# Optimization experiments

Measured on AMD Instinct MI355X. Metric: run time of the kernel, lower is better.

The kernel has to match this reference:

```python
import jax, jax.numpy as jnp
import numpy as np

N = 50000        # nodes
E = 800000       # edges (avg degree 16)
F_IN = 128       # num_node_features
HEADS = 4        # const.NUM_HEADS
CH = 32          # const.NUM_CHANNELS
CLS = 40         # num_classes
NEG_SLOPE = 0.2  # PyG GATv2Conv default


def setup_inputs() -> dict:
    key = jax.random.key(0)
    ks = jax.random.split(key, 10)
    x = jax.random.normal(ks[0], (N, F_IN), dtype=jnp.float32)
    edge_index = jax.random.randint(ks[1], (2, E), 0, N, dtype=jnp.int64)
    s1 = 1.0 / np.sqrt(F_IN)
    s2 = 1.0 / np.sqrt(HEADS * CH)
    w1_l = jax.random.normal(ks[2], (F_IN, HEADS * CH), jnp.float32) * s1
    w1_r = jax.random.normal(ks[3], (F_IN, HEADS * CH), jnp.float32) * s1
    a1 = jax.random.normal(ks[4], (HEADS, CH), jnp.float32) * (1.0 / np.sqrt(CH))
    b1 = jnp.zeros((HEADS * CH,), jnp.float32)
    w2_l = jax.random.normal(ks[5], (HEADS * CH, CLS), jnp.float32) * s2
    w2_r = jax.random.normal(ks[6], (HEADS * CH, CLS), jnp.float32) * s2
    a2 = jax.random.normal(ks[7], (1, CLS), jnp.float32) * (1.0 / np.sqrt(CLS))
    b2 = jnp.zeros((CLS,), jnp.float32)
    return {"x": x, "edge_index": edge_index, "w1_l": w1_l, "w1_r": w1_r,
            "a1": a1, "b1": b1, "w2_l": w2_l, "w2_r": w2_r, "a2": a2, "b2": b2}


def _gatv2_conv(x, src, dst, wl, wr, a, b, concat):
    """GATv2Conv (PyG semantics, eval mode: no dropout).
    src -> lin_l, dst -> lin_r; e = a . LeakyReLU(x_l[src] + x_r[dst]);
    segment softmax over dst; out_i = sum_j alpha * x_l[src]."""
    H, C = a.shape
    n = x.shape[0]
    xl = (x @ wl).reshape(n, H, C)
    xr = (x @ wr).reshape(n, H, C)
    # per-edge additive attention logits [E, H]
    e = jnp.einsum('ehc,hc->eh', jax.nn.leaky_relu(xl[src] + xr[dst], NEG_SLOPE), a)
    # numerically stable segment softmax over target nodes
    m = jax.ops.segment_max(e, dst, num_segments=n)          # [n, H]
    p = jnp.exp(e - m[dst])
    denom = jax.ops.segment_sum(p, dst, num_segments=n)     # [n, H]
    alpha = p / denom[dst]
    out = jax.ops.segment_sum(alpha[..., None] * xl[src], dst, num_segments=n)  # [n, H, C]
    out = out.reshape(n, H * C) if concat else out.mean(axis=1)
    return out + b


def reference(x, edge_index, w1_l, w1_r, a1, b1, w2_l, w2_r, a2, b2):
    n = x.shape[0]
    # PyG GATv2Conv default add_self_loops=True
    loop = jnp.arange(n, dtype=edge_index.dtype)
    src = jnp.concatenate([edge_index[0], loop])
    dst = jnp.concatenate([edge_index[1], loop])
    h = jax.nn.elu(_gatv2_conv(x, src, dst, w1_l, w1_r, a1, b1, concat=True))
    # F.dropout with training=False is identity
    out = _gatv2_conv(h, src, dst, w2_l, w2_r, a2, b2, concat=False)
    return jax.nn.log_softmax(out, axis=1)
```

## Files before the change

kernel.cpp:

```cpp
#include <hip/hip_runtime.h>
#include <hip/hip_bf16.h>
#include <math.h>

#define NN 50000
#define NE 800000
#define ETOT (NE + NN)
#define CLS 40
#define CLSP 48
#define NEG 0.2f
#define MTILES (NN / 16)
#define GB1 ((MTILES + 3) / 4)
#define PREPB 176
#define NBUCK 196
#define BCAP 8192
#define EB 4096
#define KAB ((ETOT + EB - 1) / EB)
#define NHALF (NN / 2)

#define L2E 1.44269504088896f
#define C06 (0.6f * L2E)
#define C04 (0.4f * L2E)

typedef __hip_bfloat16 bf16;
typedef __attribute__((ext_vector_type(8))) __bf16 bf16x8;
typedef __attribute__((ext_vector_type(4))) float f32x4;
typedef __attribute__((ext_vector_type(2))) float f32x2;
struct U3 { unsigned x, y, z; };

__device__ __forceinline__ bf16x8 cvt8(f32x4 a, f32x4 b) {
    bf16x8 r;
    r[0] = (__bf16)a[0]; r[1] = (__bf16)a[1]; r[2] = (__bf16)a[2]; r[3] = (__bf16)a[3];
    r[4] = (__bf16)b[0]; r[5] = (__bf16)b[1]; r[6] = (__bf16)b[2]; r[7] = (__bf16)b[3];
    return r;
}
__device__ __forceinline__ f32x2 unpk2(unsigned u) {
    f32x2 r;
    r.x = __uint_as_float(u << 16);
    r.y = __uint_as_float(u & 0xffff0000u);
    return r;
}

__device__ __forceinline__ unsigned scan256(unsigned v, unsigned* wsum) {
    int t = threadIdx.x;
    int lane = t & 63, w = t >> 6;
    unsigned inc = v;
#pragma unroll
    for (int d = 1; d < 64; d <<= 1) {
        unsigned x = __shfl_up(inc, d);
        if (lane >= d) inc += x;
    }
    if (lane == 63) wsum[w] = inc;
    __syncthreads();
    unsigned woff = 0;
#pragma unroll
    for (int i = 0; i < 4; i++) woff += (i < w) ? wsum[i] : 0;
    return woff + inc - v;
}

__global__ __launch_bounds__(256) void prep(
        const float* __restrict__ w1l, const float* __restrict__ w1r,
        const float* __restrict__ w2l, const float* __restrict__ w2r,
        bf16* __restrict__ wT1, bf16* __restrict__ wT2,
        int* __restrict__ bcursor) {
    int t = blockIdx.x * 256 + threadIdx.x;
    if (t < NBUCK) bcursor[t] = 0;
    if (t < 2 * 128 * 128) {
        int m = t >> 14;
        int idx = t & 16383;
        int n = idx >> 7, k = idx & 127;
        const float* w = m ? w1r : w1l;
        wT1[t] = __float2bfloat16(w[k * 128 + n]);
    } else if (t < 2 * 128 * 128 + 2 * CLSP * 128) {
        int u = t - 2 * 128 * 128;
        int m = u / (CLSP * 128);
        int idx = u % (CLSP * 128);
        int n = idx >> 7, k = idx & 127;
        const float* w = m ? w2r : w2l;
        wT2[u] = __float2bfloat16((n < CLS) ? w[k * CLS + n] : 0.0f);
    }
}

__global__ __launch_bounds__(256) void gemm1_scatter(
        const float* __restrict__ x, const bf16* __restrict__ wT,
        bf16* __restrict__ outL, bf16* __restrict__ outR,
        const int* __restrict__ ei, int* __restrict__ bcursor,
        uint2* __restrict__ tmp) {
    __shared__ unsigned hist[256];
    __shared__ unsigned lstart[256];
    __shared__ unsigned lcur[256];
    __shared__ unsigned gbase[256];
    __shared__ unsigned wsum[4];
    __shared__ uint2 binned[EB];
    __shared__ unsigned target[EB];
    if ((int)blockIdx.x < GB1) {
        int wave = threadIdx.x >> 6;
        int lane = threadIdx.x & 63;
        int tile = blockIdx.x * 4 + wave;
        if (tile >= MTILES) return;
        const bf16* wl = wT;
        const bf16* wr = wT + 128 * 128;
        int row0 = tile * 16;
        int l16 = lane & 15, quad = lane >> 4;
        f32x4 z = {0.f, 0.f, 0.f, 0.f};
        f32x4 accl[8], accr[8];
#pragma unroll
        for (int i = 0; i < 8; i++) { accl[i] = z; accr[i] = z; }
        const float* xrow = x + (size_t)(row0 + l16) * 128 + quad * 8;
#pragma unroll
        for (int k0 = 0; k0 < 128; k0 += 32) {
            f32x4 a0 = *reinterpret_cast<const f32x4*>(xrow + k0);
            f32x4 a1v = *reinterpret_cast<const f32x4*>(xrow + k0 + 4);
            bf16x8 a = cvt8(a0, a1v);
#pragma unroll
            for (int ct = 0; ct < 8; ct++) {
                bf16x8 bl = *reinterpret_cast<const bf16x8*>(wl + (ct * 16 + l16) * 128 + k0 + quad * 8);
                bf16x8 br = *reinterpret_cast<const bf16x8*>(wr + (ct * 16 + l16) * 128 + k0 + quad * 8);
                accl[ct] = __builtin_amdgcn_mfma_f32_16x16x32_bf16(a, bl, accl[ct], 0, 0, 0);
                accr[ct] = __builtin_amdgcn_mfma_f32_16x16x32_bf16(a, br, accr[ct], 0, 0, 0);
            }
        }
#pragma unroll
        for (int ct = 0; ct < 8; ct++)
#pragma unroll
            for (int r = 0; r < 4; r++) {
                size_t o = (size_t)(row0 + quad * 4 + r) * 128 + ct * 16 + l16;
                outL[o] = __float2bfloat16(accl[ct][r]);
                outR[o] = __float2bfloat16(accr[ct][r]);
            }
    } else {
        int t = threadIdx.x;
        int e0 = (blockIdx.x - GB1) * EB;
        hist[t] = 0;
        __syncthreads();
        int srcs[16], dsts[16];
#pragma unroll
        for (int i = 0; i < 16; i++) {
            int e = e0 + i * 256 + t;
            if (e < ETOT) {
                int s, d;
                if (e < NE) { s = ei[e]; d = ei[NE + e]; }
                else        { s = d = e - NE; }
                srcs[i] = s; dsts[i] = d;
                atomicAdd(&hist[d >> 8], 1u);
            } else dsts[i] = -1;
        }
        __syncthreads();
        unsigned v = hist[t];
        unsigned excl = scan256(v, wsum);
        lstart[t] = excl;
        lcur[t] = 0;
        __syncthreads();
        if (t < NBUCK && v > 0)
            gbase[t] = (unsigned)atomicAdd(&bcursor[t], (int)v) + (unsigned)t * BCAP;
        __syncthreads();
#pragma unroll
        for (int i = 0; i < 16; i++) {
            int d = dsts[i];
            if (d >= 0) {
                int bk = d >> 8;
                unsigned p = atomicAdd(&lcur[bk], 1u);
                unsigned slot = lstart[bk] + p;
                binned[slot] = make_uint2((unsigned)srcs[i], (unsigned)d);
                target[slot] = gbase[bk] + p;
            }
        }
        __syncthreads();
        int tot = min(EB, ETOT - e0);
        for (int s = t; s < tot; s += 256)
            tmp[target[s]] = binned[s];
    }
}

__global__ __launch_bounds__(256) void bucket_sort(const int* __restrict__ bcursor,
                                                   const uint2* __restrict__ tmp,
                                                   int* __restrict__ csr_src,
                                                   int* __restrict__ startA,
                                                   int* __restrict__ degA) {
    __shared__ unsigned hist[256];
    __shared__ unsigned lcur[256];
    __shared__ unsigned wsum[4];
    __shared__ int vals[BCAP];
    int b = blockIdx.x, t = threadIdx.x;
    int cnt = bcursor[b];
    hist[t] = 0;
    __syncthreads();
    const uint2* seg = tmp + (size_t)b * BCAP;
    for (int s = t; s < cnt; s += 256)
        atomicAdd(&hist[seg[s].y & 255], 1u);
    __syncthreads();
    unsigned v = hist[t];
    unsigned excl = scan256(v, wsum);
    lcur[t] = excl;
    int node = b * 256 + t;
    if (node < NN) {
        startA[node] = b * BCAP + (int)excl;
        degA[node] = (int)v;
    }
    __syncthreads();
    for (int s = t; s < cnt; s += 256) {
        uint2 p = seg[s];
        unsigned pos = atomicAdd(&lcur[p.y & 255], 1u);
        vals[pos] = (int)p.x;
    }
    __syncthreads();
    int* cbase = csr_src + (size_t)b * BCAP;
    for (int s = t; s < cnt; s += 256)
        cbase[s] = vals[s];
}

struct L1S { float s; f32x2 acc[4]; };
__device__ __forceinline__ void l1_consume(uint4 u, bool valid, const f32x2* xrp,
                                           const f32x2* a06, const float* a04, L1S& st) {
    f32x2 t0 = unpk2(u.x) + xrp[0];
    f32x2 t1 = unpk2(u.y) + xrp[1];
    f32x2 t2 = unpk2(u.z) + xrp[2];
    f32x2 t3 = unpk2(u.w) + xrp[3];
    f32x2 ep = t0 * a06[0];
    ep = __builtin_elementwise_fma(t1, a06[1], ep);
    ep = __builtin_elementwise_fma(t2, a06[2], ep);
    ep = __builtin_elementwise_fma(t3, a06[3], ep);
    float e0 = fmaf(a04[1], fabsf(t0.y), a04[0] * fabsf(t0.x));
    e0 = fmaf(a04[2], fabsf(t1.x), e0);
    e0 = fmaf(a04[3], fabsf(t1.y), e0);
    float e1 = fmaf(a04[5], fabsf(t2.y), a04[4] * fabsf(t2.x));
    e1 = fmaf(a04[6], fabsf(t3.x), e1);
    e1 = fmaf(a04[7], fabsf(t3.y), e1);
    float e = (ep.x + ep.y) + (e0 + e1);
    e += __shfl_xor(e, 1);
    e += __shfl_xor(e, 2);
    float w = valid ? __builtin_amdgcn_exp2f(e) : 0.f;
    st.s += w;
    f32x2 wv = {w, w};
    st.acc[0] = __builtin_elementwise_fma(wv, t0, st.acc[0]);
    st.acc[1] = __builtin_elementwise_fma(wv, t1, st.acc[1]);
    st.acc[2] = __builtin_elementwise_fma(wv, t2, st.acc[2]);
    st.acc[3] = __builtin_elementwise_fma(wv, t3, st.acc[3]);
}

__global__ __launch_bounds__(256) void node_l1(const int* __restrict__ startA,
                                               const int* __restrict__ degA,
                                               const int* __restrict__ csr_src,
                                               const bf16* __restrict__ xl,
                                               const bf16* __restrict__ xr,
                                               const float* __restrict__ a1,
                                               const float* __restrict__ b1,
                                               bf16* __restrict__ hb,
                                               int nbase) {
    int wid = nbase + ((blockIdx.x * 256 + threadIdx.x) >> 6);
    int lane = threadIdx.x & 63;
    int g = lane >> 4, t = lane & 15;
    unsigned cB = (unsigned)t * 16;
    int j0 = startA[wid];
    int deg = degA[wid];
    unsigned rowB = (unsigned)csr_src[j0 + min(lane, deg - 1)] << 8;
    const char* xlb = (const char*)xl;
    f32x2 xrp[4];
    {
        uint4 raw = *(const uint4*)((const char*)xr + ((unsigned)wid << 8) + cB);
        xrp[0] = unpk2(raw.x); xrp[1] = unpk2(raw.y);
        xrp[2] = unpk2(raw.z); xrp[3] = unpk2(raw.w);
    }
    f32x2 a06[4];
    float a04[8];
    {
        f32x4 lo = *reinterpret_cast<const f32x4*>(a1 + t * 8);
        f32x4 hi = *reinterpret_cast<const f32x4*>(a1 + t * 8 + 4);
        float af[8];
#pragma unroll
        for (int k = 0; k < 4; k++) { af[k] = lo[k]; af[k + 4] = hi[k]; }
#pragma unroll
        for (int j = 0; j < 4; j++) {
            a06[j].x = af[2 * j] * C06;
            a06[j].y = af[2 * j + 1] * C06;
        }
#pragma unroll
        for (int k = 0; k < 8; k++) a04[k] = af[k] * C04;
    }
    L1S st; st.s = 0.f;
    f32x2 z2 = {0.f, 0.f};
#pragma unroll
    for (int k = 0; k < 4; k++) st.acc[k] = z2;
    int nb = (deg + 3) >> 2;
    uint4 u[8];
#pragma unroll
    for (int i = 0; i < 4; i++) {
        int pp = min(i * 4 + g, deg - 1);
        u[i] = *(const uint4*)(xlb + (__shfl(rowB, pp) + cB));
    }
    if (nb > 4) {
#pragma unroll
        for (int i = 4; i < 8; i++) {
            int pp = min(i * 4 + g, deg - 1);
            u[i] = *(const uint4*)(xlb + (__shfl(rowB, pp) + cB));
        }
    }
    l1_consume(u[0], g < deg, xrp, a06, a04, st);
    if (nb > 1) l1_consume(u[1], 4 + g < deg, xrp, a06, a04, st);
    if (nb > 2) l1_consume(u[2], 8 + g < deg, xrp, a06, a04, st);
    if (nb > 3) l1_consume(u[3], 12 + g < deg, xrp, a06, a04, st);
    if (nb > 4) {
        l1_consume(u[4], 16 + g < deg, xrp, a06, a04, st);
        if (nb > 5) l1_consume(u[5], 20 + g < deg, xrp, a06, a04, st);
        if (nb > 6) l1_consume(u[6], 24 + g < deg, xrp, a06, a04, st);
        if (nb > 7) l1_consume(u[7], 28 + g < deg, xrp, a06, a04, st);
        for (int b = 8; b < nb; b++) {
            int p = b * 4 + g;
            bool valid = p < deg;
            int pp = valid ? p : deg - 1;
            unsigned o = __shfl(rowB, min(pp, 63)) + cB;
            if (pp >= 64) o = (((unsigned)csr_src[j0 + pp]) << 8) + cB;
            uint4 uu = *(const uint4*)(xlb + o);
            l1_consume(uu, valid, xrp, a06, a04, st);
        }
    }
#pragma unroll
    for (int d = 16; d < 64; d <<= 1) {
        st.s += __shfl_xor(st.s, d);
#pragma unroll
        for (int k = 0; k < 4; k++) {
            st.acc[k].x += __shfl_xor(st.acc[k].x, d);
            st.acc[k].y += __shfl_xor(st.acc[k].y, d);
        }
    }
    if (g == 0) {
        float inv = 1.f / st.s;
        unsigned pk[4];
#pragma unroll
        for (int k = 0; k < 4; k++) {
            float o0 = st.acc[k].x * inv - xrp[k].x + b1[t * 8 + 2 * k];
            float o1 = st.acc[k].y * inv - xrp[k].y + b1[t * 8 + 2 * k + 1];
            o0 = o0 > 0.f ? o0 : __expf(o0) - 1.f;
            o1 = o1 > 0.f ? o1 : __expf(o1) - 1.f;
            bf16 r0 = __float2bfloat16(o0), r1 = __float2bfloat16(o1);
            pk[k] = (unsigned)*reinterpret_cast<unsigned short*>(&r0) |
                    ((unsigned)*reinterpret_cast<unsigned short*>(&r1) << 16);
        }
        uint4 w4 = {pk[0], pk[1], pk[2], pk[3]};
        *(uint4*)((char*)hb + ((unsigned)wid << 8) + cB) = w4;
    }
}

__global__ __launch_bounds__(256) void gemm2(const bf16* __restrict__ h,
                                             const bf16* __restrict__ wT,
                                             bf16* __restrict__ outL,
                                             bf16* __restrict__ outR) {
    int wave = threadIdx.x >> 6;
    int lane = threadIdx.x & 63;
    int tile = blockIdx.x * 4 + wave;
    if (tile >= MTILES) return;
    const bf16* wl = wT;
    const bf16* wr = wT + CLSP * 128;
    int row0 = tile * 16;
    int l16 = lane & 15, quad = lane >> 4;
    f32x4 z = {0.f, 0.f, 0.f, 0.f};
    f32x4 accl[3], accr[3];
#pragma unroll
    for (int i = 0; i < 3; i++) { accl[i] = z; accr[i] = z; }
    const bf16* hrow = h + (size_t)(row0 + l16) * 128 + quad * 8;
#pragma unroll
    for (int k0 = 0; k0 < 128; k0 += 32) {
        bf16x8 a = *reinterpret_cast<const bf16x8*>(hrow + k0);
#pragma unroll
        for (int ct = 0; ct < 3; ct++) {
            bf16x8 bl = *reinterpret_cast<const bf16x8*>(wl + (ct * 16 + l16) * 128 + k0 + quad * 8);
            bf16x8 br = *reinterpret_cast<const bf16x8*>(wr + (ct * 16 + l16) * 128 + k0 + quad * 8);
            accl[ct] = __builtin_amdgcn_mfma_f32_16x16x32_bf16(a, bl, accl[ct], 0, 0, 0);
            accr[ct] = __builtin_amdgcn_mfma_f32_16x16x32_bf16(a, br, accr[ct], 0, 0, 0);
        }
    }
#pragma unroll
    for (int ct = 0; ct < 3; ct++)
#pragma unroll
        for (int r = 0; r < 4; r++) {
            size_t o = (size_t)(row0 + quad * 4 + r) * CLSP + ct * 16 + l16;
            outL[o] = __float2bfloat16(accl[ct][r]);
            outR[o] = __float2bfloat16(accr[ct][r]);
        }
}

struct L2S { float s; f32x2 acc[3]; };
__device__ __forceinline__ void l2_consume(U3 u, bool valid, const f32x2* xrp,
                                           const f32x2* a06, const float* a04, L2S& st) {
    f32x2 t0 = unpk2(u.x) + xrp[0];
    f32x2 t1 = unpk2(u.y) + xrp[1];
    f32x2 t2 = unpk2(u.z) + xrp[2];
    f32x2 ep = t0 * a06[0];
    ep = __builtin_elementwise_fma(t1, a06[1], ep);
    ep = __builtin_elementwise_fma(t2, a06[2], ep);
    float es = fmaf(a04[1], fabsf(t0.y), a04[0] * fabsf(t0.x));
    es = fmaf(a04[2], fabsf(t1.x), es);
    es = fmaf(a04[3], fabsf(t1.y), es);
    es = fmaf(a04[4], fabsf(t2.x), es);
    es = fmaf(a04[5], fabsf(t2.y), es);
    float e = (ep.x + ep.y) + es;
    e += __shfl_xor(e, 1);
    e += __shfl_xor(e, 2);
    e += __shfl_xor(e, 4);
    float w = valid ? __builtin_amdgcn_exp2f(e) : 0.f;
    st.s += w;
    f32x2 wv = {w, w};
    st.acc[0] = __builtin_elementwise_fma(wv, t0, st.acc[0]);
    st.acc[1] = __builtin_elementwise_fma(wv, t1, st.acc[1]);
    st.acc[2] = __builtin_elementwise_fma(wv, t2, st.acc[2]);
}

__global__ __launch_bounds__(256) void node_l2(const int* __restrict__ startA,
                                               const int* __restrict__ degA,
                                               const int* __restrict__ csr_src,
                                               const bf16* __restrict__ xl2,
                                               const bf16* __restrict__ xr2,
                                               const float* __restrict__ a2,
                                               const float* __restrict__ b2,
                                               float* __restrict__ out) {
    int wid = (blockIdx.x * 256 + threadIdx.x) >> 6;
    int lane = threadIdx.x & 63;
    int g = lane >> 3, t = lane & 7;
    unsigned cB = (unsigned)t * 12;
    int j0 = startA[wid];
    int deg = degA[wid];
    unsigned rowB = (unsigned)csr_src[j0 + min(lane, deg - 1)] * 96u;
    const char* xlb = (const char*)xl2;
    f32x2 xrp[3];
    {
        U3 raw = *(const U3*)((const char*)xr2 + (unsigned)wid * 96u + cB);
        xrp[0] = unpk2(raw.x); xrp[1] = unpk2(raw.y); xrp[2] = unpk2(raw.z);
    }
    int c = t * 6;
    f32x2 a06[3];
    float a04[6];
#pragma unroll
    for (int k = 0; k < 6; k++) {
        float av = (c + k < CLS) ? a2[c + k] : 0.f;
        a04[k] = av * C04;
        if (k & 1) a06[k >> 1].y = av * C06; else a06[k >> 1].x = av * C06;
    }
    L2S st; st.s = 0.f;
    f32x2 z2 = {0.f, 0.f};
#pragma unroll
    for (int k = 0; k < 3; k++) st.acc[k] = z2;
    int nb = (deg + 7) >> 3;
    U3 u[4];
#pragma unroll
    for (int i = 0; i < 2; i++) {
        int pp = min(i * 8 + g, deg - 1);
        u[i] = *(const U3*)(xlb + (__shfl(rowB, pp) + cB));
    }
    if (nb > 2) {
#pragma unroll
        for (int i = 2; i < 4; i++) {
            int pp = min(i * 8 + g, deg - 1);
            u[i] = *(const U3*)(xlb + (__shfl(rowB, pp) + cB));
        }
    }
    l2_consume(u[0], g < deg, xrp, a06, a04, st);
    if (nb > 1) l2_consume(u[1], 8 + g < deg, xrp, a06, a04, st);
    if (nb > 2) {
        l2_consume(u[2], 16 + g < deg, xrp, a06, a04, st);
        if (nb > 3) l2_consume(u[3], 24 + g < deg, xrp, a06, a04, st);
        for (int b = 4; b < nb; b++) {
            int p = b * 8 + g;
            bool valid = p < deg;
            int pp = valid ? p : deg - 1;
            unsigned o = __shfl(rowB, min(pp, 63)) + cB;
            if (pp >= 64) o = (unsigned)csr_src[j0 + pp] * 96u + cB;
            U3 uu = *(const U3*)(xlb + o);
            l2_consume(uu, valid, xrp, a06, a04, st);
        }
    }
#pragma unroll
    for (int d = 8; d < 64; d <<= 1) {
        st.s += __shfl_xor(st.s, d);
#pragma unroll
        for (int k = 0; k < 3; k++) {
            st.acc[k].x += __shfl_xor(st.acc[k].x, d);
            st.acc[k].y += __shfl_xor(st.acc[k].y, d);
        }
    }
    float inv = 1.f / st.s;
    float q[6];
    float mx = -3e38f;
#pragma unroll
    for (int k = 0; k < 6; k++) {
        bool val = (c + k < CLS);
        float av = (k & 1) ? st.acc[k >> 1].y : st.acc[k >> 1].x;
        float xv = (k & 1) ? xrp[k >> 1].y : xrp[k >> 1].x;
        q[k] = val ? (av * inv - xv + b2[c + k]) : -3e38f;
        mx = fmaxf(mx, q[k]);
    }
    mx = fmaxf(mx, __shfl_xor(mx, 1));
    mx = fmaxf(mx, __shfl_xor(mx, 2));
    mx = fmaxf(mx, __shfl_xor(mx, 4));
    float se = 0.f;
#pragma unroll
    for (int k = 0; k < 6; k++) if (c + k < CLS) se += __expf(q[k] - mx);
    se += __shfl_xor(se, 1);
    se += __shfl_xor(se, 2);
    se += __shfl_xor(se, 4);
    float ls = mx + __logf(se);
    if (g == 0) {
        float* o = out + (size_t)wid * CLS + c;
#pragma unroll
        for (int k = 0; k < 6; k++)
            if (c + k < CLS) o[k] = q[k] - ls;
    }
}

extern "C" void kernel_launch(void* const* d_in, const int* in_sizes, int n_in,
                              void* d_out, int out_size, void* d_ws, size_t ws_size,
                              hipStream_t stream) {
    const float* x   = (const float*)d_in[0];
    const int*   ei  = (const int*)d_in[1];
    const float* w1l = (const float*)d_in[2];
    const float* w1r = (const float*)d_in[3];
    const float* a1  = (const float*)d_in[4];
    const float* b1  = (const float*)d_in[5];
    const float* w2l = (const float*)d_in[6];
    const float* w2r = (const float*)d_in[7];
    const float* a2  = (const float*)d_in[8];
    const float* b2  = (const float*)d_in[9];
    float* out = (float*)d_out;

    char* base = (char*)d_ws;
    int*   bcursor = (int*)(base + 0);
    int*   startA  = (int*)(base + 1024);
    int*   degA    = (int*)(base + 201024);
    uint2* tmp     = (uint2*)(base + 401024);
    int*   csr_src = (int*)(base + 13246080);
    bf16*  xl1     = (bf16*)(base + 19668608);
    bf16*  hb      = (bf16*)(base + 45268608);
    bf16*  xl2p    = (bf16*)(base + 58068608);
    bf16*  wT1     = (bf16*)(base + 67668608);
    bf16*  wT2     = (bf16*)(base + 67734144);
    bf16* xr1  = xl1 + (size_t)NN * 128;
    bf16* xr2p = xl2p + (size_t)NN * CLSP;

    prep<<<PREPB, 256, 0, stream>>>(w1l, w1r, w2l, w2r, wT1, wT2, bcursor);
    gemm1_scatter<<<GB1 + KAB, 256, 0, stream>>>(x, wT1, xl1, xr1, ei, bcursor, tmp);
    bucket_sort<<<NBUCK, 256, 0, stream>>>(bcursor, tmp, csr_src, startA, degA);
    node_l1<<<(NHALF * 64) / 256, 256, 0, stream>>>(startA, degA, csr_src, xl1, xr1, a1, b1, hb, 0);
    node_l1<<<(NHALF * 64) / 256, 256, 0, stream>>>(startA, degA, csr_src, xl1, xr1, a1, b1, hb, NHALF);
    gemm2<<<GB1, 256, 0, stream>>>(hb, wT2, xl2p, xr2p);
    node_l2<<<(NN * 64) / 256, 256, 0, stream>>>(startA, degA, csr_src, xl2p, xr2p, a2, b2, out);
}
```

Baseline: 232.1 us.

## Replace bucket sort CSR build with global atomic count, scan, scatter

Replaces the two-level bucketed sort (shared-memory binning plus per-bucket local sort) with a classic CSR build: per-node atomic degree counting fused into the first GEMM launch, a single-block prefix scan, and a global-atomic scatter of source ids. This drops the large intermediate tmp buffer and the per-block shared-memory histogramming, at the cost of global atomic contention and a serial single-block scan kernel. CSR order within a node becomes nondeterministic, which may change floating-point summation order. It also splits node_l2 into two half launches.

Result: slower. 313.9 us (+35.3%).

```diff
diff --git a/kernel.cpp b/kernel.cpp
--- a/kernel.cpp
+++ b/kernel.cpp
@@ -5,16 +5,15 @@
 #define NN 50000
 #define NE 800000
 #define ETOT (NE + NN)
+#define NPAD 50176
 #define CLS 40
 #define CLSP 48
 #define NEG 0.2f
 #define MTILES (NN / 16)
 #define GB1 ((MTILES + 3) / 4)
-#define PREPB 176
-#define NBUCK 196
-#define BCAP 8192
-#define EB 4096
-#define KAB ((ETOT + EB - 1) / EB)
+#define PREPB 196
+#define CNTB 196
+#define SCB 208
 #define NHALF (NN / 2)
 
 #define L2E 1.44269504088896f
@@ -61,9 +60,9 @@
         const float* __restrict__ w1l, const float* __restrict__ w1r,
         const float* __restrict__ w2l, const float* __restrict__ w2r,
         bf16* __restrict__ wT1, bf16* __restrict__ wT2,
-        int* __restrict__ bcursor) {
+        int* __restrict__ degA) {
     int t = blockIdx.x * 256 + threadIdx.x;
-    if (t < NBUCK) bcursor[t] = 0;
+    if (t < NPAD) degA[t] = (t < NN) ? 1 : 0;
     if (t < 2 * 128 * 128) {
         int m = t >> 14;
         int idx = t & 16383;
@@ -80,18 +79,10 @@
     }
 }
 
-__global__ __launch_bounds__(256) void gemm1_scatter(
+__global__ __launch_bounds__(256) void gemm1_count(
         const float* __restrict__ x, const bf16* __restrict__ wT,
         bf16* __restrict__ outL, bf16* __restrict__ outR,
-        const int* __restrict__ ei, int* __restrict__ bcursor,
-        uint2* __restrict__ tmp) {
-    __shared__ unsigned hist[256];
-    __shared__ unsigned lstart[256];
-    __shared__ unsigned lcur[256];
-    __shared__ unsigned gbase[256];
-    __shared__ unsigned wsum[4];
-    __shared__ uint2 binned[EB];
-    __shared__ unsigned target[EB];
+        const int* __restrict__ ei, int* __restrict__ degA) {
     if ((int)blockIdx.x < GB1) {
         int wave = threadIdx.x >> 6;
         int lane = threadIdx.x & 63;
@@ -129,83 +120,59 @@
             }
     } else {
         int t = threadIdx.x;
-        int e0 = (blockIdx.x - GB1) * EB;
-        hist[t] = 0;
-        __syncthreads();
-        int srcs[16], dsts[16];
+        int e0 = ((int)blockIdx.x - GB1) * 4096;
 #pragma unroll
         for (int i = 0; i < 16; i++) {
             int e = e0 + i * 256 + t;
-            if (e < ETOT) {
-                int s, d;
-                if (e < NE) { s = ei[e]; d = ei[NE + e]; }
-                else        { s = d = e - NE; }
-                srcs[i] = s; dsts[i] = d;
-                atomicAdd(&hist[d >> 8], 1u);
-            } else dsts[i] = -1;
-        }
-        __syncthreads();
-        unsigned v = hist[t];
-        unsigned excl = scan256(v, wsum);
-        lstart[t] = excl;
-        lcur[t] = 0;
-        __syncthreads();
-        if (t < NBUCK && v > 0)
-            gbase[t] = (unsigned)atomicAdd(&bcursor[t], (int)v) + (unsigned)t * BCAP;
-        __syncthreads();
-#pragma unroll
-        for (int i = 0; i < 16; i++) {
-            int d = dsts[i];
-            if (d >= 0) {
-                int bk = d >> 8;
-                unsigned p = atomicAdd(&lcur[bk], 1u);
-                unsigned slot = lstart[bk] + p;
-                binned[slot] = make_uint2((unsigned)srcs[i], (unsigned)d);
-                target[slot] = gbase[bk] + p;
-            }
-        }
-        __syncthreads();
-        int tot = min(EB, ETOT - e0);
-        for (int s = t; s < tot; s += 256)
-            tmp[target[s]] = binned[s];
-    }
-}
-
-__global__ __launch_bounds__(256) void bucket_sort(const int* __restrict__ bcursor,
-                                                   const uint2* __restrict__ tmp,
-                                                   int* __restrict__ csr_src,
-                                                   int* __restrict__ startA,
-                                                   int* __restrict__ degA) {
-    __shared__ unsigned hist[256];
-    __shared__ unsigned lcur[256];
+            if (e < NE) atomicAdd(&degA[ei[NE + e]], 1);
+        }
+    }
+}
+
+__global__ __launch_bounds__(256) void scan_deg(const int* __restrict__ degA,
+                                                int* __restrict__ startA,
+                                                int* __restrict__ cursor) {
     __shared__ unsigned wsum[4];
-    __shared__ int vals[BCAP];
-    int b = blockIdx.x, t = threadIdx.x;
-    int cnt = bcursor[b];
-    hist[t] = 0;
-    __syncthreads();
-    const uint2* seg = tmp + (size_t)b * BCAP;
-    for (int s = t; s < cnt; s += 256)
-        atomicAdd(&hist[seg[s].y & 255], 1u);
-    __syncthreads();
-    unsigned v = hist[t];
-    unsigned excl = scan256(v, wsum);
-    lcur[t] = excl;
-    int node = b * 256 + t;
-    if (node < NN) {
-        startA[node] = b * BCAP + (int)excl;
-        degA[node] = (int)v;
-    }
-    __syncthreads();
-    for (int s = t; s < cnt; s += 256) {
-        uint2 p = seg[s];
-        unsigned pos = atomicAdd(&lcur[p.y & 255], 1u);
-        vals[pos] = (int)p.x;
-    }
-    __syncthreads();
-    int* cbase = csr_src + (size_t)b * BCAP;
-    for (int s = t; s < cnt; s += 256)
-        cbase[s] = vals[s];
+    int t = threadIdx.x;
+    const int4* d4 = reinterpret_cast<const int4*>(degA) + t * 49;
+    int s = 0;
+#pragma unroll 7
+    for (int i = 0; i < 49; i++) {
+        int4 v = d4[i];
+        s += v.x + v.y + v.z + v.w;
+    }
+    int run = (int)scan256((unsigned)s, wsum);
+    int4* s4 = reinterpret_cast<int4*>(startA) + t * 49;
+    int4* c4 = reinterpret_cast<int4*>(cursor) + t * 49;
+#pragma unroll 7
+    for (int i = 0; i < 49; i++) {
+        int4 v = d4[i];
+        int4 o;
+        o.x = run; run += v.x;
+        o.y = run; run += v.y;
+        o.z = run; run += v.z;
+        o.w = run; run += v.w;
+        s4[i] = o;
+        c4[i] = o;
+    }
+}
+
+__global__ __launch_bounds__(256) void scatter(const int* __restrict__ ei,
+                                               int* __restrict__ cursor,
+                                               int* __restrict__ csr_src) {
+    int t = threadIdx.x;
+    int e0 = blockIdx.x * 4096;
+#pragma unroll
+    for (int i = 0; i < 16; i++) {
+        int e = e0 + i * 256 + t;
+        if (e < ETOT) {
+            int s, d;
+            if (e < NE) { s = ei[e]; d = ei[NE + e]; }
+            else        { s = d = e - NE; }
+            int pos = atomicAdd(&cursor[d], 1);
+            csr_src[pos] = s;
+        }
+    }
 }
 
 struct L1S { float s; f32x2 acc[4]; };
@@ -411,8 +378,9 @@
                                                const bf16* __restrict__ xr2,
                                                const float* __restrict__ a2,
                                                const float* __restrict__ b2,
-                                               float* __restrict__ out) {
-    int wid = (blockIdx.x * 256 + threadIdx.x) >> 6;
+                                               float* __restrict__ out,
+                                               int nbase) {
+    int wid = nbase + ((blockIdx.x * 256 + threadIdx.x) >> 6);
     int lane = threadIdx.x & 63;
     int g = lane >> 3, t = lane & 7;
     unsigned cB = (unsigned)t * 12;
@@ -521,24 +489,25 @@
     float* out = (float*)d_out;
 
     char* base = (char*)d_ws;
-    int*   bcursor = (int*)(base + 0);
-    int*   startA  = (int*)(base + 1024);
-    int*   degA    = (int*)(base + 201024);
-    uint2* tmp     = (uint2*)(base + 401024);
-    int*   csr_src = (int*)(base + 13246080);
-    bf16*  xl1     = (bf16*)(base + 19668608);
-    bf16*  hb      = (bf16*)(base + 45268608);
-    bf16*  xl2p    = (bf16*)(base + 58068608);
-    bf16*  wT1     = (bf16*)(base + 67668608);
-    bf16*  wT2     = (bf16*)(base + 67734144);
+    int*   startA  = (int*)(base + 0);
+    int*   degA    = (int*)(base + 200704);
+    int*   cursor  = (int*)(base + 401408);
+    int*   csr_src = (int*)(base + 602112);
+    bf16*  xl1     = (bf16*)(base + 4002112);
+    bf16*  hb      = (bf16*)(base + 29602112);
+    bf16*  xl2p    = (bf16*)(base + 42402112);
+    bf16*  wT1     = (bf16*)(base + 52002112);
+    bf16*  wT2     = (bf16*)(base + 52067648);
     bf16* xr1  = xl1 + (size_t)NN * 128;
     bf16* xr2p = xl2p + (size_t)NN * CLSP;
 
-    prep<<<PREPB, 256, 0, stream>>>(w1l, w1r, w2l, w2r, wT1, wT2, bcursor);
-    gemm1_scatter<<<GB1 + KAB, 256, 0, stream>>>(x, wT1, xl1, xr1, ei, bcursor, tmp);
-    bucket_sort<<<NBUCK, 256, 0, stream>>>(bcursor, tmp, csr_src, startA, degA);
+    prep<<<PREPB, 256, 0, stream>>>(w1l, w1r, w2l, w2r, wT1, wT2, degA);
+    gemm1_count<<<GB1 + CNTB, 256, 0, stream>>>(x, wT1, xl1, xr1, ei, degA);
+    scan_deg<<<1, 256, 0, stream>>>(degA, startA, cursor);
+    scatter<<<SCB, 256, 0, stream>>>(ei, cursor, csr_src);
     node_l1<<<(NHALF * 64) / 256, 256, 0, stream>>>(startA, degA, csr_src, xl1, xr1, a1, b1, hb, 0);
     node_l1<<<(NHALF * 64) / 256, 256, 0, stream>>>(startA, degA, csr_src, xl1, xr1, a1, b1, hb, NHALF);
     gemm2<<<GB1, 256, 0, stream>>>(hb, wT2, xl2p, xr2p);
-    node_l2<<<(NN * 64) / 256, 256, 0, stream>>>(startA, degA, csr_src, xl2p, xr2p, a2, b2, out);
-}
+    node_l2<<<(NHALF * 64) / 256, 256, 0, stream>>>(startA, degA, csr_src, xl2p, xr2p, a2, b2, out, 0);
+    node_l2<<<(NHALF * 64) / 256, 256, 0, stream>>>(startA, degA, csr_src, xl2p, xr2p, a2, b2, out, NHALF);
+}
```
